# Performance work log

Measured on AMD Instinct MI355X. Metric: run time of the kernel, lower is better.

Reference implementation:

```python
import jax, jax.numpy as jnp
import numpy as np

N = 2_000_000
FEAT = 32


def setup_inputs() -> dict:
    key = jax.random.key(0)
    ks = jax.random.split(key, 11)
    return {
        "positions": jax.random.normal(ks[0], (N, 3), jnp.float32) * 0.1,
        "scales": jax.random.normal(ks[1], (N, 3), jnp.float32) * 0.3 - 2.0,  # log-scales ~ -2
        "rotations": jax.random.normal(ks[2], (N, 4), jnp.float32),
        "opacity": jax.random.normal(ks[3], (N, 1), jnp.float32) - 2.0,
        "features": jax.random.normal(ks[4], (N, FEAT), jnp.float32) * 0.01,
        "w1": jax.random.normal(ks[5], (FEAT, 64), jnp.float32) * (1.0 / np.sqrt(FEAT)),
        "b1": jax.random.normal(ks[6], (64,), jnp.float32) * 0.01,
        "w2": jax.random.normal(ks[7], (64, 32), jnp.float32) * (1.0 / 8.0),
        "b2": jax.random.normal(ks[8], (32,), jnp.float32) * 0.01,
        "w3": jax.random.normal(ks[9], (32, 3), jnp.float32) * (1.0 / np.sqrt(32.0)),
        "b3": jax.random.normal(ks[10], (3,), jnp.float32) * 0.01,
    }


def _quat_to_rotmat(q):
    # q: [N,4] normalized quaternion (w,x,y,z) -> [N,3,3]
    w, x, y, z = q[:, 0], q[:, 1], q[:, 2], q[:, 3]
    r00 = 1 - 2 * (y * y + z * z)
    r01 = 2 * (x * y - w * z)
    r02 = 2 * (x * z + w * y)
    r10 = 2 * (x * y + w * z)
    r11 = 1 - 2 * (x * x + z * z)
    r12 = 2 * (y * z - w * x)
    r20 = 2 * (x * z - w * y)
    r21 = 2 * (y * z + w * x)
    r22 = 1 - 2 * (x * x + y * y)
    return jnp.stack(
        [jnp.stack([r00, r01, r02], -1),
         jnp.stack([r10, r11, r12], -1),
         jnp.stack([r20, r21, r22], -1)], axis=1)


def _forward(positions, scales, rotations, opacity, features, w1, b1, w2, b2, w3, b3):
    n = positions.shape[0]
    s = jnp.exp(scales)                                   # [N,3]
    q = rotations / jnp.linalg.norm(rotations, axis=1, keepdims=True)  # F.normalize
    R = _quat_to_rotmat(q)                                # [N,3,3]
    RS = R * s[:, None, :]                                # R @ diag(s): scale columns
    cov = jnp.einsum("nij,nkj->nik", RS, RS)             # RS @ RS^T, [N,3,3]
    op = jax.nn.sigmoid(opacity)                          # [N,1]
    # shader MLP: Linear-ReLU-Linear-ReLU-Linear-Sigmoid
    h = jax.nn.relu(features @ w1 + b1)
    h = jax.nn.relu(h @ w2 + b2)
    colors = jax.nn.sigmoid(h @ w3 + b3)                  # [N,3]
    # pack get_active_parameters() outputs: positions, scales, rotations, opacity, colors, covariance
    return jnp.concatenate(
        [positions, s, q, op, colors, cov.reshape(n, 9)], axis=1)  # [N,23]


def reference(positions, scales, rotations, opacity, features, w1, b1, w2, b2, w3, b3):
    return _forward(positions, scales, rotations, opacity, features, w1, b1, w2, b2, w3, b3)
```

## Files before the change

### kernel.cpp

```cpp
#include <hip/hip_runtime.h>
#include <math.h>

#define BLOCK 256

__device__ __forceinline__ void geom_one(int idx, bool valid, int n,
                                         const float* __restrict__ positions,
                                         const float* __restrict__ scales,
                                         const float* __restrict__ rotations,
                                         const float* __restrict__ opacity,
                                         float* __restrict__ out)
{
    const size_t base = (size_t)(valid ? idx : (n - 1));

    const float px = positions[base * 3 + 0];
    const float py = positions[base * 3 + 1];
    const float pz = positions[base * 3 + 2];

    const float s0 = __expf(scales[base * 3 + 0]);
    const float s1 = __expf(scales[base * 3 + 1]);
    const float s2 = __expf(scales[base * 3 + 2]);

    float qw = rotations[base * 4 + 0];
    float qx = rotations[base * 4 + 1];
    float qy = rotations[base * 4 + 2];
    float qz = rotations[base * 4 + 3];
    const float inv = rsqrtf(qw * qw + qx * qx + qy * qy + qz * qz);
    qw *= inv; qx *= inv; qy *= inv; qz *= inv;

    float op = opacity[base];
    op = 1.0f / (1.0f + __expf(-op));

    const float r00 = 1.0f - 2.0f * (qy * qy + qz * qz);
    const float r01 = 2.0f * (qx * qy - qw * qz);
    const float r02 = 2.0f * (qx * qz + qw * qy);
    const float r10 = 2.0f * (qx * qy + qw * qz);
    const float r11 = 1.0f - 2.0f * (qx * qx + qz * qz);
    const float r12 = 2.0f * (qy * qz - qw * qx);
    const float r20 = 2.0f * (qx * qz - qw * qy);
    const float r21 = 2.0f * (qy * qz + qw * qx);
    const float r22 = 1.0f - 2.0f * (qx * qx + qy * qy);

    const float v0 = s0 * s0, v1 = s1 * s1, v2 = s2 * s2;
    const float c00 = r00 * r00 * v0 + r01 * r01 * v1 + r02 * r02 * v2;
    const float c01 = r00 * r10 * v0 + r01 * r11 * v1 + r02 * r12 * v2;
    const float c02 = r00 * r20 * v0 + r01 * r21 * v1 + r02 * r22 * v2;
    const float c11 = r10 * r10 * v0 + r11 * r11 * v1 + r12 * r12 * v2;
    const float c12 = r10 * r20 * v0 + r11 * r21 * v1 + r12 * r22 * v2;
    const float c22 = r20 * r20 * v0 + r21 * r21 * v1 + r22 * r22 * v2;

    if (valid) {
        float* __restrict__ o = out + (size_t)idx * 23;
        o[0]  = px; o[1]  = py; o[2]  = pz;
        o[3]  = s0; o[4]  = s1; o[5]  = s2;
        o[6]  = qw; o[7]  = qx; o[8]  = qy; o[9] = qz;
        o[10] = op;
        o[14] = c00; o[15] = c01; o[16] = c02;
        o[17] = c01; o[18] = c11; o[19] = c12;
        o[20] = c02; o[21] = c12; o[22] = c22;
    }
}

__global__ __launch_bounds__(BLOCK, 2)
void gsplat_fused_kernel(const float* __restrict__ positions,
                         const float* __restrict__ scales,
                         const float* __restrict__ rotations,
                         const float* __restrict__ opacity,
                         const float* __restrict__ features,
                         const float* __restrict__ w1, const float* __restrict__ b1,
                         const float* __restrict__ w2, const float* __restrict__ b2,
                         const float* __restrict__ w3, const float* __restrict__ b3,
                         float* __restrict__ out, int n)
{
    __shared__ float sw1t[64 * 32];
    __shared__ float sw2[64 * 32];
    __shared__ float sw3t[3 * 32];
    __shared__ float sb1[64];
    __shared__ float sb2[32];
    __shared__ float sb3[3];

    for (int t = threadIdx.x; t < 2048; t += BLOCK) {
        int i = t >> 6, j = t & 63;
        sw1t[j * 32 + i] = w1[t];
    }
    for (int t = threadIdx.x; t < 2048; t += BLOCK) sw2[t] = w2[t];
    for (int t = threadIdx.x; t < 96; t += BLOCK) {
        int k = t / 3, m = t - 3 * k;
        sw3t[m * 32 + k] = w3[t];
    }
    if (threadIdx.x < 64) sb1[threadIdx.x] = b1[threadIdx.x];
    if (threadIdx.x < 32) sb2[threadIdx.x] = b2[threadIdx.x];
    if (threadIdx.x < 3)  sb3[threadIdx.x] = b3[threadIdx.x];
    __syncthreads();

    const int pA = blockIdx.x * (BLOCK * 2) + threadIdx.x;
    const int pB = pA + BLOCK;
    const bool vA = pA < n;
    const bool vB = pB < n;

    geom_one(pA, vA, n, positions, scales, rotations, opacity, out);
    geom_one(pB, vB, n, positions, scales, rotations, opacity, out);

    const size_t bA = (size_t)(vA ? pA : (n - 1));
    const size_t bB = (size_t)(vB ? pB : (n - 1));

    float fA[32], fB[32];
    {
        const float4* fpA = (const float4*)(features + bA * 32);
        const float4* fpB = (const float4*)(features + bB * 32);
        #pragma unroll
        for (int u = 0; u < 8; ++u) {
            const float4 a = fpA[u];
            fA[u * 4 + 0] = a.x; fA[u * 4 + 1] = a.y;
            fA[u * 4 + 2] = a.z; fA[u * 4 + 3] = a.w;
            const float4 b = fpB[u];
            fB[u * 4 + 0] = b.x; fB[u * 4 + 1] = b.y;
            fB[u * 4 + 2] = b.z; fB[u * 4 + 3] = b.w;
        }
    }

    float hA[32], hB[32];
    #pragma unroll
    for (int k = 0; k < 32; ++k) { float b = sb2[k]; hA[k] = b; hB[k] = b; }

    for (int j = 0; j < 64; ++j) {
        const float* __restrict__ wc = &sw1t[j * 32];
        const float bj = sb1[j];
        float a0 = bj,   a1 = 0.0f, a2 = 0.0f, a3 = 0.0f;
        float e0 = bj,   e1 = 0.0f, e2 = 0.0f, e3 = 0.0f;
        #pragma unroll
        for (int i = 0; i < 8; ++i) {
            const float w0 = wc[i * 4 + 0], w1v = wc[i * 4 + 1];
            const float w2v = wc[i * 4 + 2], w3v = wc[i * 4 + 3];
            a0 = fmaf(fA[i * 4 + 0], w0,  a0);
            a1 = fmaf(fA[i * 4 + 1], w1v, a1);
            a2 = fmaf(fA[i * 4 + 2], w2v, a2);
            a3 = fmaf(fA[i * 4 + 3], w3v, a3);
            e0 = fmaf(fB[i * 4 + 0], w0,  e0);
            e1 = fmaf(fB[i * 4 + 1], w1v, e1);
            e2 = fmaf(fB[i * 4 + 2], w2v, e2);
            e3 = fmaf(fB[i * 4 + 3], w3v, e3);
        }
        const float h1A = fmaxf((a0 + a1) + (a2 + a3), 0.0f);
        const float h1B = fmaxf((e0 + e1) + (e2 + e3), 0.0f);

        const float* __restrict__ w2r = &sw2[j * 32];
        #pragma unroll
        for (int k = 0; k < 32; ++k) {
            const float w = w2r[k];
            hA[k] = fmaf(h1A, w, hA[k]);
            hB[k] = fmaf(h1B, w, hB[k]);
        }
    }

    float cA0 = sb3[0], cA1 = sb3[1], cA2 = sb3[2];
    float cB0 = sb3[0], cB1 = sb3[1], cB2 = sb3[2];
    #pragma unroll
    for (int k = 0; k < 32; ++k) {
        const float w0 = sw3t[k], w1v = sw3t[32 + k], w2v = sw3t[64 + k];
        const float a = fmaxf(hA[k], 0.0f);
        const float b = fmaxf(hB[k], 0.0f);
        cA0 = fmaf(a, w0, cA0); cA1 = fmaf(a, w1v, cA1); cA2 = fmaf(a, w2v, cA2);
        cB0 = fmaf(b, w0, cB0); cB1 = fmaf(b, w1v, cB1); cB2 = fmaf(b, w2v, cB2);
    }

    if (vA) {
        float* __restrict__ o = out + (size_t)pA * 23;
        o[11] = 1.0f / (1.0f + __expf(-cA0));
        o[12] = 1.0f / (1.0f + __expf(-cA1));
        o[13] = 1.0f / (1.0f + __expf(-cA2));
    }
    if (vB) {
        float* __restrict__ o = out + (size_t)pB * 23;
        o[11] = 1.0f / (1.0f + __expf(-cB0));
        o[12] = 1.0f / (1.0f + __expf(-cB1));
        o[13] = 1.0f / (1.0f + __expf(-cB2));
    }
}

extern "C" void kernel_launch(void* const* d_in, const int* in_sizes, int n_in,
                              void* d_out, int out_size, void* d_ws, size_t ws_size,
                              hipStream_t stream) {
    const float* positions = (const float*)d_in[0];
    const float* scales    = (const float*)d_in[1];
    const float* rotations = (const float*)d_in[2];
    const float* opacity   = (const float*)d_in[3];
    const float* features  = (const float*)d_in[4];
    const float* w1        = (const float*)d_in[5];
    const float* b1        = (const float*)d_in[6];
    const float* w2        = (const float*)d_in[7];
    const float* b2        = (const float*)d_in[8];
    const float* w3        = (const float*)d_in[9];
    const float* b3        = (const float*)d_in[10];
    float* out = (float*)d_out;

    const int n = in_sizes[0] / 3;
    const int grid = (n + BLOCK * 2 - 1) / (BLOCK * 2);
    gsplat_fused_kernel<<<grid, BLOCK, 0, stream>>>(
        positions, scales, rotations, opacity, features,
        w1, b1, w2, b2, w3, b3, out, n);
}
```

Baseline: 621.9 us.

## Compute shader MLP with bf16 MFMA tiles and prepacked weight fragments

Replaces the per-thread scalar FP32 MLP with bf16 16x16x32 MFMA instructions, processing 16 points per wave step. A small pre-kernel packs w1/w2/w3 into MFMA operand layout in the workspace. Intermediate activations are staged through per-wave LDS buffers, and the kernel now handles one point per thread with higher occupancy. The aim is to remove the FMA-bound MLP cost so the kernel becomes memory-bound, at the cost of bf16 precision on features and activations and an extra kernel launch.

```diff
diff --git a/kernel.cpp b/kernel.cpp
--- a/kernel.cpp
+++ b/kernel.cpp
@@ -1,179 +1,202 @@
 #include <hip/hip_runtime.h>
+#include <hip/hip_bf16.h>
 #include <math.h>
 
 #define BLOCK 256
 
-__device__ __forceinline__ void geom_one(int idx, bool valid, int n,
-                                         const float* __restrict__ positions,
-                                         const float* __restrict__ scales,
-                                         const float* __restrict__ rotations,
-                                         const float* __restrict__ opacity,
-                                         float* __restrict__ out)
+typedef __attribute__((ext_vector_type(8))) short bf16x8;
+typedef __attribute__((ext_vector_type(4))) float f32x4;
+
+static __device__ __forceinline__ short f2bf(float x) {
+    __hip_bfloat16 h = __float2bfloat16(x);
+    short s;
+    __builtin_memcpy(&s, &h, 2);
+    return s;
+}
+
+__global__ void gsplat_pack_weights(const float* __restrict__ w1,
+                                    const float* __restrict__ w2,
+                                    const float* __restrict__ w3,
+                                    ushort* __restrict__ ws)
 {
-    const size_t base = (size_t)(valid ? idx : (n - 1));
-
-    const float px = positions[base * 3 + 0];
-    const float py = positions[base * 3 + 1];
-    const float pz = positions[base * 3 + 2];
-
-    const float s0 = __expf(scales[base * 3 + 0]);
-    const float s1 = __expf(scales[base * 3 + 1]);
-    const float s2 = __expf(scales[base * 3 + 2]);
-
-    float qw = rotations[base * 4 + 0];
-    float qx = rotations[base * 4 + 1];
-    float qy = rotations[base * 4 + 2];
-    float qz = rotations[base * 4 + 3];
-    const float inv = rsqrtf(qw * qw + qx * qx + qy * qy + qz * qz);
-    qw *= inv; qx *= inv; qy *= inv; qz *= inv;
-
-    float op = opacity[base];
-    op = 1.0f / (1.0f + __expf(-op));
-
-    const float r00 = 1.0f - 2.0f * (qy * qy + qz * qz);
-    const float r01 = 2.0f * (qx * qy - qw * qz);
-    const float r02 = 2.0f * (qx * qz + qw * qy);
-    const float r10 = 2.0f * (qx * qy + qw * qz);
-    const float r11 = 1.0f - 2.0f * (qx * qx + qz * qz);
-    const float r12 = 2.0f * (qy * qz - qw * qx);
-    const float r20 = 2.0f * (qx * qz - qw * qy);
-    const float r21 = 2.0f * (qy * qz + qw * qx);
-    const float r22 = 1.0f - 2.0f * (qx * qx + qy * qy);
-
-    const float v0 = s0 * s0, v1 = s1 * s1, v2 = s2 * s2;
-    const float c00 = r00 * r00 * v0 + r01 * r01 * v1 + r02 * r02 * v2;
-    const float c01 = r00 * r10 * v0 + r01 * r11 * v1 + r02 * r12 * v2;
-    const float c02 = r00 * r20 * v0 + r01 * r21 * v1 + r02 * r22 * v2;
-    const float c11 = r10 * r10 * v0 + r11 * r11 * v1 + r12 * r12 * v2;
-    const float c12 = r10 * r20 * v0 + r11 * r21 * v1 + r12 * r22 * v2;
-    const float c22 = r20 * r20 * v0 + r21 * r21 * v1 + r22 * r22 * v2;
-
-    if (valid) {
-        float* __restrict__ o = out + (size_t)idx * 23;
-        o[0]  = px; o[1]  = py; o[2]  = pz;
-        o[3]  = s0; o[4]  = s1; o[5]  = s2;
-        o[6]  = qw; o[7]  = qx; o[8]  = qy; o[9] = qz;
-        o[10] = op;
-        o[14] = c00; o[15] = c01; o[16] = c02;
-        o[17] = c01; o[18] = c11; o[19] = c12;
-        o[20] = c02; o[21] = c12; o[22] = c22;
-    }
-}
-
-__global__ __launch_bounds__(BLOCK, 2)
-void gsplat_fused_kernel(const float* __restrict__ positions,
-                         const float* __restrict__ scales,
-                         const float* __restrict__ rotations,
-                         const float* __restrict__ opacity,
-                         const float* __restrict__ features,
-                         const float* __restrict__ w1, const float* __restrict__ b1,
-                         const float* __restrict__ w2, const float* __restrict__ b2,
-                         const float* __restrict__ w3, const float* __restrict__ b3,
-                         float* __restrict__ out, int n)
+    const int tid = threadIdx.x;
+    for (int u = tid; u < 2048; u += BLOCK) {
+        const int e = u & 7, lane = (u >> 3) & 63, ht = u >> 9;
+        const int k = (lane >> 4) * 8 + e;
+        const int j = ht * 16 + (lane & 15);
+        ws[u] = (ushort)f2bf(w1[k * 64 + j]);
+    }
+    for (int u = tid; u < 2048; u += BLOCK) {
+        const int e = u & 7, lane = (u >> 3) & 63, c = u >> 9;
+        const int kt = c >> 1, jt = c & 1;
+        const int k = kt * 32 + (lane >> 4) * 8 + e;
+        const int j = jt * 16 + (lane & 15);
+        ws[2048 + u] = (ushort)f2bf(w2[k * 32 + j]);
+    }
+    for (int u = tid; u < 512; u += BLOCK) {
+        const int e = u & 7, lane = u >> 3;
+        const int col = lane & 15;
+        const int k = (lane >> 4) * 8 + e;
+        ws[4096 + u] = (ushort)f2bf(col < 3 ? w3[k * 3 + col] : 0.0f);
+    }
+}
+
+__global__ __launch_bounds__(BLOCK, 4)
+void gsplat_mfma_kernel(const float* __restrict__ positions,
+                        const float* __restrict__ scales,
+                        const float* __restrict__ rotations,
+                        const float* __restrict__ opacity,
+                        const float* __restrict__ features,
+                        const ushort* __restrict__ wpack,
+                        const float* __restrict__ b1,
+                        const float* __restrict__ b2,
+                        const float* __restrict__ b3,
+                        float* __restrict__ out, int n)
 {
-    __shared__ float sw1t[64 * 32];
-    __shared__ float sw2[64 * 32];
-    __shared__ float sw3t[3 * 32];
-    __shared__ float sb1[64];
-    __shared__ float sb2[32];
-    __shared__ float sb3[3];
-
-    for (int t = threadIdx.x; t < 2048; t += BLOCK) {
-        int i = t >> 6, j = t & 63;
-        sw1t[j * 32 + i] = w1[t];
-    }
-    for (int t = threadIdx.x; t < 2048; t += BLOCK) sw2[t] = w2[t];
-    for (int t = threadIdx.x; t < 96; t += BLOCK) {
-        int k = t / 3, m = t - 3 * k;
-        sw3t[m * 32 + k] = w3[t];
-    }
-    if (threadIdx.x < 64) sb1[threadIdx.x] = b1[threadIdx.x];
-    if (threadIdx.x < 32) sb2[threadIdx.x] = b2[threadIdx.x];
-    if (threadIdx.x < 3)  sb3[threadIdx.x] = b3[threadIdx.x];
-    __syncthreads();
-
-    const int pA = blockIdx.x * (BLOCK * 2) + threadIdx.x;
-    const int pB = pA + BLOCK;
-    const bool vA = pA < n;
-    const bool vB = pB < n;
-
-    geom_one(pA, vA, n, positions, scales, rotations, opacity, out);
-    geom_one(pB, vB, n, positions, scales, rotations, opacity, out);
-
-    const size_t bA = (size_t)(vA ? pA : (n - 1));
-    const size_t bB = (size_t)(vB ? pB : (n - 1));
-
-    float fA[32], fB[32];
+    __shared__ __align__(16) ushort lds[4 * 1792];
+
+    const int tid  = threadIdx.x;
+    const int wave = tid >> 6;
+    const int lane = tid & 63;
+    const int lrow = lane & 15;
+    const int lkg  = lane >> 4;
+
+    const int blockBase = blockIdx.x * BLOCK;
+
     {
-        const float4* fpA = (const float4*)(features + bA * 32);
-        const float4* fpB = (const float4*)(features + bB * 32);
-        #pragma unroll
-        for (int u = 0; u < 8; ++u) {
-            const float4 a = fpA[u];
-            fA[u * 4 + 0] = a.x; fA[u * 4 + 1] = a.y;
-            fA[u * 4 + 2] = a.z; fA[u * 4 + 3] = a.w;
-            const float4 b = fpB[u];
-            fB[u * 4 + 0] = b.x; fB[u * 4 + 1] = b.y;
-            fB[u * 4 + 2] = b.z; fB[u * 4 + 3] = b.w;
+        const int pt = blockBase + tid;
+        if (pt < n) {
+            const size_t base = (size_t)pt;
+            const float px = positions[base * 3 + 0];
+            const float py = positions[base * 3 + 1];
+            const float pz = positions[base * 3 + 2];
+
+            const float s0 = __expf(scales[base * 3 + 0]);
+            const float s1 = __expf(scales[base * 3 + 1]);
+            const float s2 = __expf(scales[base * 3 + 2]);
+
+            float qw = rotations[base * 4 + 0];
+            float qx = rotations[base * 4 + 1];
+            float qy = rotations[base * 4 + 2];
+            float qz = rotations[base * 4 + 3];
+            const float inv = rsqrtf(qw * qw + qx * qx + qy * qy + qz * qz);
+            qw *= inv; qx *= inv; qy *= inv; qz *= inv;
+
+            float op = opacity[base];
+            op = 1.0f / (1.0f + __expf(-op));
+
+            const float r00 = 1.0f - 2.0f * (qy * qy + qz * qz);
+            const float r01 = 2.0f * (qx * qy - qw * qz);
+            const float r02 = 2.0f * (qx * qz + qw * qy);
+            const float r10 = 2.0f * (qx * qy + qw * qz);
+            const float r11 = 1.0f - 2.0f * (qx * qx + qz * qz);
+            const float r12 = 2.0f * (qy * qz - qw * qx);
+            const float r20 = 2.0f * (qx * qz - qw * qy);
+            const float r21 = 2.0f * (qy * qz + qw * qx);
+            const float r22 = 1.0f - 2.0f * (qx * qx + qy * qy);
+
+            const float v0 = s0 * s0, v1 = s1 * s1, v2 = s2 * s2;
+            const float c00 = r00 * r00 * v0 + r01 * r01 * v1 + r02 * r02 * v2;
+            const float c01 = r00 * r10 * v0 + r01 * r11 * v1 + r02 * r12 * v2;
+            const float c02 = r00 * r20 * v0 + r01 * r21 * v1 + r02 * r22 * v2;
+            const float c11 = r10 * r10 * v0 + r11 * r11 * v1 + r12 * r12 * v2;
+            const float c12 = r10 * r20 * v0 + r11 * r21 * v1 + r12 * r22 * v2;
+            const float c22 = r20 * r20 * v0 + r21 * r21 * v1 + r22 * r22 * v2;
+
+            float* __restrict__ o = out + base * 23;
+            o[0]  = px; o[1]  = py; o[2]  = pz;
+            o[3]  = s0; o[4]  = s1; o[5]  = s2;
+            o[6]  = qw; o[7]  = qx; o[8]  = qy; o[9] = qz;
+            o[10] = op;
+            o[14] = c00; o[15] = c01; o[16] = c02;
+            o[17] = c01; o[18] = c11; o[19] = c12;
+            o[20] = c02; o[21] = c12; o[22] = c22;
         }
     }
 
-    float hA[32], hB[32];
-    #pragma unroll
-    for (int k = 0; k < 32; ++k) { float b = sb2[k]; hA[k] = b; hB[k] = b; }
-
-    for (int j = 0; j < 64; ++j) {
-        const float* __restrict__ wc = &sw1t[j * 32];
-        const float bj = sb1[j];
-        float a0 = bj,   a1 = 0.0f, a2 = 0.0f, a3 = 0.0f;
-        float e0 = bj,   e1 = 0.0f, e2 = 0.0f, e3 = 0.0f;
-        #pragma unroll
-        for (int i = 0; i < 8; ++i) {
-            const float w0 = wc[i * 4 + 0], w1v = wc[i * 4 + 1];
-            const float w2v = wc[i * 4 + 2], w3v = wc[i * 4 + 3];
-            a0 = fmaf(fA[i * 4 + 0], w0,  a0);
-            a1 = fmaf(fA[i * 4 + 1], w1v, a1);
-            a2 = fmaf(fA[i * 4 + 2], w2v, a2);
-            a3 = fmaf(fA[i * 4 + 3], w3v, a3);
-            e0 = fmaf(fB[i * 4 + 0], w0,  e0);
-            e1 = fmaf(fB[i * 4 + 1], w1v, e1);
-            e2 = fmaf(fB[i * 4 + 2], w2v, e2);
-            e3 = fmaf(fB[i * 4 + 3], w3v, e3);
+    const bf16x8* wp = (const bf16x8*)wpack;
+    bf16x8 w1f[4];
+    #pragma unroll
+    for (int ht = 0; ht < 4; ++ht) w1f[ht] = wp[ht * 64 + lane];
+    bf16x8 w2f[2][2];
+    #pragma unroll
+    for (int kt = 0; kt < 2; ++kt)
+        #pragma unroll
+        for (int jt = 0; jt < 2; ++jt)
+            w2f[kt][jt] = wp[256 + (kt * 2 + jt) * 64 + lane];
+    const bf16x8 w3f = wp[512 + lane];
+
+    float b1v[4];
+    #pragma unroll
+    for (int ht = 0; ht < 4; ++ht) b1v[ht] = b1[ht * 16 + lrow];
+    float b2v[2];
+    #pragma unroll
+    for (int jt = 0; jt < 2; ++jt) b2v[jt] = b2[jt * 16 + lrow];
+    const float b3v = (lrow < 3) ? b3[lrow] : 0.0f;
+
+    ushort* h1 = &lds[wave * 1792];
+    ushort* h2 = h1 + 1152;
+
+    const int waveBase = blockBase + wave * 64;
+    const f32x4 zero = {0.0f, 0.0f, 0.0f, 0.0f};
+
+    for (int p = 0; p < 4; ++p) {
+        const int pt0 = waveBase + p * 16;
+
+        int ptA = pt0 + lrow;
+        if (ptA >= n) ptA = n - 1;
+        const float* fsrc = features + (size_t)ptA * 32 + lkg * 8;
+        const float4 fa = *(const float4*)(fsrc);
+        const float4 fb = *(const float4*)(fsrc + 4);
+        bf16x8 a1;
+        a1[0] = f2bf(fa.x); a1[1] = f2bf(fa.y); a1[2] = f2bf(fa.z); a1[3] = f2bf(fa.w);
+        a1[4] = f2bf(fb.x); a1[5] = f2bf(fb.y); a1[6] = f2bf(fb.z); a1[7] = f2bf(fb.w);
+
+        f32x4 c1[4];
+        #pragma unroll
+        for (int ht = 0; ht < 4; ++ht)
+            c1[ht] = __builtin_amdgcn_mfma_f32_16x16x32_bf16(a1, w1f[ht], zero, 0, 0, 0);
+
+        const int h1w = (lkg * 4) * 72 + lrow;
+        #pragma unroll
+        for (int ht = 0; ht < 4; ++ht)
+            #pragma unroll
+            for (int r = 0; r < 4; ++r)
+                h1[h1w + r * 72 + ht * 16] =
+                    (ushort)f2bf(fmaxf(c1[ht][r] + b1v[ht], 0.0f));
+
+        const bf16x8* h1r = (const bf16x8*)(h1 + lrow * 72);
+        const bf16x8 a2lo = h1r[lkg];
+        const bf16x8 a2hi = h1r[4 + lkg];
+
+        f32x4 c2[2];
+        #pragma unroll
+        for (int jt = 0; jt < 2; ++jt) {
+            f32x4 acc = __builtin_amdgcn_mfma_f32_16x16x32_bf16(a2lo, w2f[0][jt], zero, 0, 0, 0);
+            c2[jt]    = __builtin_amdgcn_mfma_f32_16x16x32_bf16(a2hi, w2f[1][jt], acc, 0, 0, 0);
         }
-        const float h1A = fmaxf((a0 + a1) + (a2 + a3), 0.0f);
-        const float h1B = fmaxf((e0 + e1) + (e2 + e3), 0.0f);
-
-        const float* __restrict__ w2r = &sw2[j * 32];
-        #pragma unroll
-        for (int k = 0; k < 32; ++k) {
-            const float w = w2r[k];
-            hA[k] = fmaf(h1A, w, hA[k]);
-            hB[k] = fmaf(h1B, w, hB[k]);
+
+        const int h2w = (lkg * 4) * 40 + lrow;
+        #pragma unroll
+        for (int jt = 0; jt < 2; ++jt)
+            #pragma unroll
+            for (int r = 0; r < 4; ++r)
+                h2[h2w + r * 40 + jt * 16] =
+                    (ushort)f2bf(fmaxf(c2[jt][r] + b2v[jt], 0.0f));
+
+        const bf16x8* h2r = (const bf16x8*)(h2 + lrow * 40);
+        const bf16x8 a3 = h2r[lkg];
+        const f32x4 c3 = __builtin_amdgcn_mfma_f32_16x16x32_bf16(a3, w3f, zero, 0, 0, 0);
+
+        if (lrow < 3) {
+            #pragma unroll
+            for (int r = 0; r < 4; ++r) {
+                const int pt = pt0 + lkg * 4 + r;
+                if (pt < n)
+                    out[(size_t)pt * 23 + 11 + lrow] =
+                        1.0f / (1.0f + __expf(-(c3[r] + b3v)));
+            }
         }
-    }
-
-    float cA0 = sb3[0], cA1 = sb3[1], cA2 = sb3[2];
-    float cB0 = sb3[0], cB1 = sb3[1], cB2 = sb3[2];
-    #pragma unroll
-    for (int k = 0; k < 32; ++k) {
-        const float w0 = sw3t[k], w1v = sw3t[32 + k], w2v = sw3t[64 + k];
-        const float a = fmaxf(hA[k], 0.0f);
-        const float b = fmaxf(hB[k], 0.0f);
-        cA0 = fmaf(a, w0, cA0); cA1 = fmaf(a, w1v, cA1); cA2 = fmaf(a, w2v, cA2);
-        cB0 = fmaf(b, w0, cB0); cB1 = fmaf(b, w1v, cB1); cB2 = fmaf(b, w2v, cB2);
-    }
-
-    if (vA) {
-        float* __restrict__ o = out + (size_t)pA * 23;
-        o[11] = 1.0f / (1.0f + __expf(-cA0));
-        o[12] = 1.0f / (1.0f + __expf(-cA1));
-        o[13] = 1.0f / (1.0f + __expf(-cA2));
-    }
-    if (vB) {
-        float* __restrict__ o = out + (size_t)pB * 23;
-        o[11] = 1.0f / (1.0f + __expf(-cB0));
-        o[12] = 1.0f / (1.0f + __expf(-cB1));
-        o[13] = 1.0f / (1.0f + __expf(-cB2));
     }
 }
 
@@ -193,9 +216,13 @@
     const float* b3        = (const float*)d_in[10];
     float* out = (float*)d_out;
 
+    ushort* wpack = (ushort*)d_ws;
+
+    gsplat_pack_weights<<<1, BLOCK, 0, stream>>>(w1, w2, w3, wpack);
+
     const int n = in_sizes[0] / 3;
-    const int grid = (n + BLOCK * 2 - 1) / (BLOCK * 2);
-    gsplat_fused_kernel<<<grid, BLOCK, 0, stream>>>(
+    const int grid = (n + BLOCK - 1) / BLOCK;
+    gsplat_mfma_kernel<<<grid, BLOCK, 0, stream>>>(
         positions, scales, rotations, opacity, features,
-        w1, b1, w2, b2, w3, b3, out, n);
-}
+        wpack, b1, b2, b3, out, n);
+}
```

New measurement: 549.8 us. 11.6% less time.
